# Kernel tuning notes

Measured on AMD Instinct MI355X. Metric: run time of the kernel, lower is better.

The kernel has to match this reference:

```python
import jax, jax.numpy as jnp
import numpy as np

B, L, K, D, V = 512, 50, 32, 100, 100000


def setup_inputs() -> dict:
    key = jax.random.key(0)
    ks = jax.random.split(key, 32)
    g = lambda i, shape, s=0.1: jax.random.normal(ks[i], shape, jnp.float32) * s
    lens = jax.random.randint(ks[0], (B,), 1, L + 1)
    seq = jax.random.randint(ks[1], (B, L), 1, V)
    seq = jnp.where(jnp.arange(L)[None, :] < lens[:, None], seq, 0)  # pad past lens with 0
    nei = jax.random.randint(ks[2], (B, K), 1, V)
    wei = jax.random.uniform(ks[3], (B, K), jnp.float32)
    s_vec = g(4, (B, D), 1.0)
    zp = lambda E: E.at[0].set(0.0)  # padding_idx=0
    return {
        'seq': seq, 'lens': lens, 'nei': nei, 'wei': wei, 's_vec': s_vec,
        'E_tag': zp(g(5, (V, D))), 'E_ggnn': zp(g(6, (V, D))), 'E_glob': zp(g(7, (V, D))),
        'W_ih': g(8, (2 * D, 3 * D)), 'b_ih': g(9, (3 * D,)),
        'W_hh': g(10, (D, 3 * D)), 'b_hh': g(11, (3 * D,)),
        'Wout_w': g(12, (D, D)), 'Wout_b': g(13, (D,)),
        'W_w': g(14, (D, D)),
        'W3_w': g(15, (3 * D, D)), 'W3_b': g(16, (D,)),
        'W1_w': g(17, (D + 1, D)), 'W1_b': g(18, (D,)),
        'q1_w': g(19, (D,)),
        'W2_w': g(20, (2 * D, D)), 'W2_b': g(21, (D,)),
        'G1_w': g(22, (D + 1, D)), 'G1_b': g(23, (D,)),
        'G2_w': g(24, (D, 1)), 'G2_b': g(25, (1,)),
    }


def _forward(seq, lens, nei, wei, s_vec, E_tag, E_ggnn, E_glob, W_ih, b_ih, W_hh, b_hh,
             Wout_w, Wout_b, W_w, W3_w, W3_b, W1_w, W1_b, q1_w, W2_w, W2_b,
             G1_w, G1_b, G2_w, G2_b):
    Bv, Lv = seq.shape
    # --- TAGNN_Base: vectorized chain adjacency (edges i->i+1 for i < lens-1, plus identity) ---
    i = jnp.arange(Lv - 1)
    edge = (i[None, :] < (lens - 1)[:, None]).astype(jnp.float32)  # [B, L-1]
    eye = jnp.eye(Lv, dtype=jnp.float32)[None]
    z3 = jnp.zeros((Bv, Lv, Lv), jnp.float32)
    adj_out = z3.at[:, i, i + 1].set(edge) + eye
    adj_in = z3.at[:, i + 1, i].set(edge) + eye
    # --- GGNN: one propagation step + GRUCell ---
    x = E_ggnn[seq]  # [B, L, D]
    a = jnp.concatenate([jnp.einsum('bij,bjd->bid', adj_out, x),
                         jnp.einsum('bij,bjd->bid', adj_in, x)], -1)  # [B, L, 2D]
    gi = a @ W_ih + b_ih
    gh = x @ W_hh + b_hh
    ir, iz, ig = jnp.split(gi, 3, -1)
    hr, hz, hg = jnp.split(gh, 3, -1)
    r = jax.nn.sigmoid(ir + hr)
    zt = jax.nn.sigmoid(iz + hz)
    n = jnp.tanh(ig + r * hg)
    h = (1.0 - zt) * n + zt * x
    h = h @ Wout_w + Wout_b  # [B, L, D]
    # --- target-aware attention readout ---
    mask = (seq > 0).astype(jnp.float32)
    bi = jnp.arange(Bv)
    h_last = h[bi, lens - 1]
    target = seq[bi, lens - 1]
    t_emb = E_tag[target]
    att = jax.nn.softmax(jnp.sum(h * (t_emb @ W_w)[:, None, :], -1), -1)
    h_glb = jnp.sum(h * att[..., None] * mask[..., None], 1)
    sess = jnp.tanh(jnp.concatenate([h_glb, h_last, t_emb], -1) @ W3_w + W3_b)
    logits_base = sess @ E_tag.T  # [B, V]
    # --- GlobalEncoder (2 layers); nei/wei are layer-invariant so attention msg is too ---
    h_nei = E_glob[nei]  # [B, K, D]
    feat = jnp.concatenate([h_nei * s_vec[:, None, :], wei[..., None]], -1)  # [B, K, D+1]
    score = jnp.tanh(feat @ W1_w + W1_b) @ q1_w  # [B, K]
    attg = jax.nn.softmax(score, -1)
    msg = jnp.sum(attg[..., None] * h_nei, 1)  # [B, D]
    xg = E_glob[target]
    for _ in range(2):
        xg = jax.nn.relu(jnp.concatenate([xg, msg], -1) @ W2_w + W2_b)
    # pos_emb[:, 0, :] is the scalar (L-1)/L, so h_global is scaled by 1/L
    xg = xg * (1.0 - (Lv - 1) / Lv)
    # --- gating between base logits mean and global rep ---
    mean_b = jnp.mean(logits_base, 1, keepdims=True)  # [B, 1]
    gate_in = jnp.concatenate([mean_b, xg], -1)  # [B, D+1]
    gate = jax.nn.sigmoid(jnp.tanh(gate_in @ G1_w + G1_b) @ G2_w + G2_b)  # [B, 1]
    sess2 = gate * xg + (1.0 - gate) * mean_b  # [B, D]
    return sess2 @ E_tag.T  # [B, V]


def reference(seq, lens, nei, wei, s_vec, E_tag, E_ggnn, E_glob, W_ih, b_ih, W_hh, b_hh,
              Wout_w, Wout_b, W_w, W3_w, W3_b, W1_w, W1_b, q1_w, W2_w, W2_b,
              G1_w, G1_b, G2_w, G2_b):
    return _forward(seq, lens, nei, wei, s_vec, E_tag, E_ggnn, E_glob, W_ih, b_ih, W_hh,
                    b_hh, Wout_w, Wout_b, W_w, W3_w, W3_b, W1_w, W1_b, q1_w, W2_w, W2_b,
                    G1_w, G1_b, G2_w, G2_b)
```

## Files before the change

kernel.cpp:

```cpp
#include <hip/hip_runtime.h>
#include <math.h>

namespace {
constexpr int NB = 512;
constexpr int NL = 50;
constexpr int NKN = 32;
constexpr int ND = 100;
constexpr int NV = 100000;
constexpr int NBL = NB * NL;
constexpr int NVP = 100096;
constexpr int NEB = 1564;
}

typedef __attribute__((ext_vector_type(8))) short bf16x8;
typedef __attribute__((ext_vector_type(4))) short short4v;
typedef __attribute__((ext_vector_type(8))) short short8v;
typedef __attribute__((ext_vector_type(4))) float f32x4;

__device__ inline unsigned short f2bf(float x) {
    unsigned u = __float_as_uint(x);
    unsigned r = (u + 0x7fffu + ((u >> 16) & 1u)) >> 16;
    return (unsigned short)r;
}
__device__ inline float bf2f(unsigned short h) {
    return __uint_as_float(((unsigned)h) << 16);
}

__global__ __launch_bounds__(256) void prep_E(
    const float* __restrict__ E_tag,
    unsigned short* __restrict__ Efrag,
    float* __restrict__ partialT)
{
    __shared__ float es[64][100];
    const int tid = threadIdx.x;
    const int blk = blockIdx.x;
    const int v0  = blk * 64;

    for (int idx = tid; idx < 1600; idx += 256) {
        size_t base = (size_t)v0 * 100 + (size_t)idx * 4;
        float4 e = make_float4(0.f, 0.f, 0.f, 0.f);
        if (base + 3 < (size_t)NV * ND) e = *(const float4*)(E_tag + base);
        int row = idx / 25, c4 = (idx - row * 25) * 4;
        es[row][c4]     = e.x;
        es[row][c4 + 1] = e.y;
        es[row][c4 + 2] = e.z;
        es[row][c4 + 3] = e.w;
    }
    __syncthreads();

    if (tid < ND) {
        float a = 0.f;
#pragma unroll 8
        for (int rr = 0; rr < 64; ++rr) a += es[rr][tid];
        partialT[(size_t)tid * NEB + blk] = a;
    }

    for (int idx = tid; idx < 16 * 64; idx += 256) {
        int kg = idx >> 6, vloc = idx & 63;
        short8v o;
#pragma unroll
        for (int j = 0; j < 8; ++j) {
            int k = kg * 8 + j;
            o[j] = (short)((k < ND) ? f2bf(es[vloc][k]) : 0);
        }
        *(short8v*)(Efrag + ((size_t)kg * NVP + v0 + vloc) * 8) = o;
    }
}

__global__ __launch_bounds__(256) void ebar_final(const float* __restrict__ partialT,
                                                  float* __restrict__ ebar)
{
    const int d = blockIdx.x;
    const int tid = threadIdx.x;
    float a = 0.f;
    for (int i = tid; i < NEB; i += 256) a += partialT[(size_t)d * NEB + i];
#pragma unroll
    for (int off = 32; off > 0; off >>= 1) a += __shfl_down(a, off);
    __shared__ float wsum[4];
    if ((tid & 63) == 0) wsum[tid >> 6] = a;
    __syncthreads();
    if (tid == 0)
        ebar[d] = (wsum[0] + wsum[1] + wsum[2] + wsum[3]) * (1.f / (float)NV);
}

__global__ __launch_bounds__(256) void prep_A(
    const int* __restrict__ seq, const int* __restrict__ lens,
    const float* __restrict__ E_ggnn, unsigned short* __restrict__ Afrag)
{
    __shared__ float xs[34][100];
    __shared__ float eo_s[34], ei_s[34];
    const int tid = threadIdx.x;
    const int r0  = blockIdx.x * 32;

    for (int idx = tid; idx < 34 * 25; idx += 256) {
        int row = idx / 25, qq = idx - row * 25;
        int rg = r0 - 1 + row;
        rg = rg < 0 ? 0 : (rg >= NBL ? NBL - 1 : rg);
        float4 e = *(const float4*)(E_ggnn + (size_t)seq[rg] * ND + 4 * qq);
        xs[row][4 * qq]     = e.x;
        xs[row][4 * qq + 1] = e.y;
        xs[row][4 * qq + 2] = e.z;
        xs[row][4 * qq + 3] = e.w;
    }
    for (int rr = tid; rr < 34; rr += 256) {
        int rg = r0 - 1 + rr;
        int rc = rg < 0 ? 0 : (rg >= NBL ? NBL - 1 : rg);
        int b = rc / NL, l = rc - b * NL;
        int lenb = lens[b];
        eo_s[rr] = (l < lenb - 1) ? 1.f : 0.f;
        ei_s[rr] = (l >= 1 && l <= lenb - 1) ? 1.f : 0.f;
    }
    __syncthreads();

    for (int idx = tid; idx < 32 * 48; idx += 256) {
        int rloc = idx / 48, kg = idx - rloc * 48;
        int seg = kg >> 4, kk = kg & 15;
        short8v o;
        float eo = eo_s[1 + rloc], ei = ei_s[1 + rloc];
#pragma unroll
        for (int j = 0; j < 8; ++j) {
            int k = kk * 8 + j;
            float v = 0.f;
            if (k < 100) {
                if (seg == 0)      v = xs[1 + rloc][k] + eo * xs[2 + rloc][k];
                else if (seg == 1) v = xs[1 + rloc][k] + ei * xs[rloc][k];
                else               v = xs[1 + rloc][k];
            }
            o[j] = (short)f2bf(v);
        }
        *(short8v*)(Afrag + ((size_t)kg * NBL + r0 + rloc) * 8) = o;
    }
}

__global__ __launch_bounds__(256) void prep_B(
    const float* __restrict__ W_ih, const float* __restrict__ W_hh,
    unsigned short* __restrict__ Bfrag)
{
    int idx = blockIdx.x * 256 + threadIdx.x;
    if (idx >= 48 * 640) return;
    int kg = idx / 640, col = idx - kg * 640;
    int seg = kg >> 4, kk = kg & 15;
    short8v o;
#pragma unroll
    for (int j = 0; j < 8; ++j) {
        int k = kk * 8 + j;
        float v = 0.f;
        if (k < 100) {
            if (seg == 0 && col < 300)                 v = W_ih[k * 300 + col];
            else if (seg == 1 && col < 300)            v = W_ih[(100 + k) * 300 + col];
            else if (seg == 2 && col >= 300 && col < 600) v = W_hh[k * 300 + (col - 300)];
        }
        o[j] = (short)f2bf(v);
    }
    *(short8v*)(Bfrag + (size_t)idx * 8) = o;
}

__global__ __launch_bounds__(256) void gates_mfma(
    const unsigned short* __restrict__ Afrag,
    const unsigned short* __restrict__ Bfrag,
    unsigned short* __restrict__ G)
{
    const int tid = threadIdx.x;
    const int r0  = blockIdx.x * 128;
    const int v0  = blockIdx.y * 128;
    const int lane = tid & 63;
    const int wv = tid >> 6;
    const int wm = wv >> 1, wn = wv & 1;
    const int q = lane >> 4, c = lane & 15;

    f32x4 acc[4][4];
#pragma unroll
    for (int fm = 0; fm < 4; ++fm)
#pragma unroll
        for (int fn = 0; fn < 4; ++fn) acc[fm][fn] = (f32x4)0.f;

    const bf16x8* Ap = (const bf16x8*)Afrag;
    const bf16x8* Bp = (const bf16x8*)Bfrag;

#pragma unroll
    for (int s = 0; s < 12; ++s) {
        const int kg = 4 * s + q;
        bf16x8 a[4], b[4];
#pragma unroll
        for (int fm = 0; fm < 4; ++fm)
            a[fm] = Ap[(size_t)kg * NBL + r0 + wm * 64 + fm * 16 + c];
#pragma unroll
        for (int fn = 0; fn < 4; ++fn)
            b[fn] = Bp[(size_t)kg * 640 + v0 + wn * 64 + fn * 16 + c];
#pragma unroll
        for (int fm = 0; fm < 4; ++fm)
#pragma unroll
            for (int fn = 0; fn < 4; ++fn)
                acc[fm][fn] = __builtin_amdgcn_mfma_f32_16x16x32_bf16(
                    a[fm], b[fn], acc[fm][fn], 0, 0, 0);
    }

#pragma unroll
    for (int fm = 0; fm < 4; ++fm) {
        int rb = r0 + wm * 64 + fm * 16 + q * 4;
#pragma unroll
        for (int fn = 0; fn < 4; ++fn) {
            int col = v0 + wn * 64 + fn * 16 + c;
            if (col < 600) {
#pragma unroll
                for (int r = 0; r < 4; ++r)
                    G[(size_t)(rb + r) * 600 + col] = f2bf(acc[fm][fn][r]);
            }
        }
    }
}

__global__ __launch_bounds__(256) void gru2(
    const int* __restrict__ seq, const float* __restrict__ E_ggnn,
    const unsigned short* __restrict__ G,
    const float* __restrict__ b_ih, const float* __restrict__ b_hh,
    float* __restrict__ h0)
{
    int idx = blockIdx.x * 256 + threadIdx.x;
    if (idx >= NBL * ND) return;
    int r = idx / ND, d = idx - r * ND;
    const unsigned short* Gr = G + (size_t)r * 600;
    float ir = bf2f(Gr[d])       + b_ih[d];
    float iz = bf2f(Gr[100 + d]) + b_ih[100 + d];
    float ig = bf2f(Gr[200 + d]) + b_ih[200 + d];
    float hr = bf2f(Gr[300 + d]) + b_hh[d];
    float hz = bf2f(Gr[400 + d]) + b_hh[100 + d];
    float hg = bf2f(Gr[500 + d]) + b_hh[200 + d];
    float x  = E_ggnn[(size_t)seq[r] * ND + d];
    float rg = 1.f / (1.f + expf(-(ir + hr)));
    float zg = 1.f / (1.f + expf(-(iz + hz)));
    float ng = tanhf(ig + rg * hg);
    h0[idx] = (1.f - zg) * ng + zg * x;
}

__global__ __launch_bounds__(128) void fuse_kernel(
    const int* __restrict__ seq, const int* __restrict__ lens,
    const int* __restrict__ nei, const float* __restrict__ wei,
    const float* __restrict__ s_vec, const float* __restrict__ E_tag,
    const float* __restrict__ E_glob,
    const float* __restrict__ Wout_w, const float* __restrict__ Wout_b,
    const float* __restrict__ W_w,
    const float* __restrict__ W3_w, const float* __restrict__ W3_b,
    const float* __restrict__ W1_w, const float* __restrict__ W1_b,
    const float* __restrict__ q1_w,
    const float* __restrict__ W2_w, const float* __restrict__ W2_b,
    const float* __restrict__ G1_w, const float* __restrict__ G1_b,
    const float* __restrict__ G2_w, const float* __restrict__ G2_b,
    const float* __restrict__ ebar, const float* __restrict__ h0,
    unsigned short* __restrict__ A_hi)
{
    const int b = blockIdx.x, tid = threadIdx.x;
    __shared__ float t_emb[100], tw[100], twW[100], red[128];
    __shared__ float al[50], att[50];
    __shared__ float g0[100], cc[300], sess_s[100];
    __shared__ float sv[100], hnei[32][100], msg[100], xg[100], xg2[100];
    __shared__ float attg[32], score[32];
    __shared__ float scalars[4];

    int lenb   = lens[b];
    int last_r = b * NL + (lenb - 1);
    int target = seq[last_r];

    if (tid < ND) {
        t_emb[tid] = E_tag[(size_t)target * ND + tid];
        sv[tid]    = s_vec[b * ND + tid];
    }
    __syncthreads();

    if (tid < ND) {
        float a = 0.f;
        for (int k = 0; k < ND; ++k) a += t_emb[k] * W_w[k * ND + tid];
        tw[tid] = a;
    }
    __syncthreads();

    if (tid < ND) {
        float a = 0.f;
        for (int d = 0; d < ND; ++d) a += Wout_w[tid * ND + d] * tw[d];
        twW[tid] = a;
    }
    red[tid] = (tid < ND) ? Wout_b[tid] * tw[tid] : 0.f;
    __syncthreads();
    for (int s = 64; s > 0; s >>= 1) { if (tid < s) red[tid] += red[tid + s]; __syncthreads(); }
    if (tid == 0) scalars[0] = red[0];
    __syncthreads();

    if (tid < NL) {
        const float* hr = h0 + (size_t)(b * NL + tid) * ND;
        float a = scalars[0];
        for (int k = 0; k < ND; ++k) a += hr[k] * twW[k];
        al[tid] = a;
    }
    __syncthreads();
    if (tid == 0) {
        float m = -1e30f;
        for (int l = 0; l < NL; ++l) m = fmaxf(m, al[l]);
        float s = 0.f;
        for (int l = 0; l < NL; ++l) { float e = expf(al[l] - m); att[l] = e; s += e; }
        float inv = 1.f / s, sm = 0.f;
        for (int l = 0; l < NL; ++l) { att[l] *= inv; if (l < lenb) sm += att[l]; }
        scalars[1] = sm;
    }
    __syncthreads();

    if (tid < ND) {
        float a = 0.f;
        for (int l = 0; l < lenb; ++l) a += att[l] * h0[(size_t)(b * NL + l) * ND + tid];
        g0[tid] = a;
    }
    __syncthreads();
    if (tid < ND) {
        float hg = 0.f, hl = 0.f;
        const float* hlast = h0 + (size_t)last_r * ND;
        for (int k = 0; k < ND; ++k) {
            float w = Wout_w[k * ND + tid];
            hg += g0[k] * w;
            hl += hlast[k] * w;
        }
        cc[tid]        = hg + scalars[1] * Wout_b[tid];
        cc[100 + tid]  = hl + Wout_b[tid];
        cc[200 + tid]  = t_emb[tid];
    }
    __syncthreads();

    if (tid < ND) {
        float a = W3_b[tid];
        for (int j = 0; j < 300; ++j) a += cc[j] * W3_w[j * ND + tid];
        sess_s[tid] = tanhf(a);
    }
    __syncthreads();
    red[tid] = (tid < ND) ? sess_s[tid] * ebar[tid] : 0.f;
    __syncthreads();
    for (int s = 64; s > 0; s >>= 1) { if (tid < s) red[tid] += red[tid + s]; __syncthreads(); }
    if (tid == 0) scalars[2] = red[0];
    __syncthreads();

    for (int idx = tid; idx < NKN * ND; idx += 128) {
        int k = idx / ND, d = idx - k * ND;
        hnei[k][d] = E_glob[(size_t)nei[b * NKN + k] * ND + d];
    }
    __syncthreads();

    {
        const int wv = tid >> 6, lane = tid & 63;
        for (int k2 = 0; k2 < NKN / 2; ++k2) {
            int k = k2 * 2 + wv;
            float p = 0.f;
            if (lane < 50) {
                float wk = wei[b * NKN + k];
                float a0 = W1_b[lane]      + wk * W1_w[100 * ND + lane];
                float a1 = W1_b[lane + 50] + wk * W1_w[100 * ND + lane + 50];
                for (int j = 0; j < ND; ++j) {
                    float t = hnei[k][j] * sv[j];
                    a0 += t * W1_w[j * ND + lane];
                    a1 += t * W1_w[j * ND + lane + 50];
                }
                p = tanhf(a0) * q1_w[lane] + tanhf(a1) * q1_w[lane + 50];
            }
            for (int off = 32; off > 0; off >>= 1) p += __shfl_down(p, off);
            if (lane == 0) score[k] = p;
        }
    }
    __syncthreads();

    if (tid == 0) {
        float m = -1e30f;
        for (int k = 0; k < NKN; ++k) m = fmaxf(m, score[k]);
        float s = 0.f;
        for (int k = 0; k < NKN; ++k) { float e = expf(score[k] - m); attg[k] = e; s += e; }
        float inv = 1.f / s;
        for (int k = 0; k < NKN; ++k) attg[k] *= inv;
    }
    __syncthreads();
    if (tid < ND) {
        float a = 0.f;
        for (int k = 0; k < NKN; ++k) a += attg[k] * hnei[k][tid];
        msg[tid] = a;
        xg[tid]  = E_glob[(size_t)target * ND + tid];
    }
    __syncthreads();
    if (tid < ND) {
        float a = W2_b[tid];
        for (int j = 0; j < ND; ++j) a += xg[j]  * W2_w[j * ND + tid];
        for (int j = 0; j < ND; ++j) a += msg[j] * W2_w[(100 + j) * ND + tid];
        xg2[tid] = fmaxf(a, 0.f);
    }
    __syncthreads();
    const float SCALE = (float)(1.0 - 49.0 / 50.0);
    if (tid < ND) {
        float a = W2_b[tid];
        for (int j = 0; j < ND; ++j) a += xg2[j] * W2_w[j * ND + tid];
        for (int j = 0; j < ND; ++j) a += msg[j] * W2_w[(100 + j) * ND + tid];
        xg[tid] = fmaxf(a, 0.f) * SCALE;
    }
    __syncthreads();

    if (tid < ND) {
        float a = G1_b[tid] + scalars[2] * G1_w[tid];
        for (int j = 0; j < ND; ++j) a += xg[j] * G1_w[(1 + j) * ND + tid];
        red[tid] = tanhf(a) * G2_w[tid];
    } else red[tid] = 0.f;
    __syncthreads();
    for (int s = 64; s > 0; s >>= 1) { if (tid < s) red[tid] += red[tid + s]; __syncthreads(); }
    if (tid == 0) scalars[3] = 1.f / (1.f + expf(-(red[0] + G2_b[0])));
    __syncthreads();

    {
        float val = 0.f;
        if (tid < ND) {
            float g = scalars[3];
            val = g * xg[tid] + (1.f - g) * scalars[2];
        }
        int kgrp = tid >> 3, j = tid & 7;
        A_hi[kgrp * 4096 + b * 8 + j] = f2bf(val);
    }
}

__global__ __launch_bounds__(256) void out_gemm_mfma(
    const unsigned short* __restrict__ A_hi,
    const unsigned short* __restrict__ Efrag,
    float* __restrict__ out)
{
    const int tid = threadIdx.x;
    const int v0  = blockIdx.x * 128;
    const int b0  = blockIdx.y * 128;
    const int lane = tid & 63;
    const int wv = tid >> 6;
    const int wm = wv >> 1, wn = wv & 1;
    const int q = lane >> 4, c = lane & 15;

    f32x4 acc[4][4];
#pragma unroll
    for (int fm = 0; fm < 4; ++fm)
#pragma unroll
        for (int fn = 0; fn < 4; ++fn) acc[fm][fn] = (f32x4)0.f;

    const bf16x8* Ah = (const bf16x8*)A_hi;
    const bf16x8* Ef = (const bf16x8*)Efrag;

#pragma unroll
    for (int s = 0; s < 4; ++s) {
        const int kg = 4 * s + q;
        bf16x8 a[4], b[4];
#pragma unroll
        for (int fm = 0; fm < 4; ++fm)
            a[fm] = Ah[kg * 512 + b0 + wm * 64 + fm * 16 + c];
#pragma unroll
        for (int fn = 0; fn < 4; ++fn)
            b[fn] = Ef[(size_t)kg * NVP + v0 + wn * 64 + fn * 16 + c];
#pragma unroll
        for (int fm = 0; fm < 4; ++fm)
#pragma unroll
            for (int fn = 0; fn < 4; ++fn)
                acc[fm][fn] = __builtin_amdgcn_mfma_f32_16x16x32_bf16(
                    a[fm], b[fn], acc[fm][fn], 0, 0, 0);
    }

#pragma unroll
    for (int fm = 0; fm < 4; ++fm) {
        int row_base = b0 + wm * 64 + fm * 16 + q * 4;
#pragma unroll
        for (int fn = 0; fn < 4; ++fn) {
            int col = v0 + wn * 64 + fn * 16 + c;
            if (col < NV) {
#pragma unroll
                for (int r = 0; r < 4; ++r)
                    out[(size_t)(row_base + r) * NV + col] = acc[fm][fn][r];
            }
        }
    }
}

extern "C" void kernel_launch(void* const* d_in, const int* in_sizes, int n_in,
                              void* d_out, int out_size, void* d_ws, size_t ws_size,
                              hipStream_t stream)
{
    const int*   seq    = (const int*)  d_in[0];
    const int*   lens   = (const int*)  d_in[1];
    const int*   nei    = (const int*)  d_in[2];
    const float* wei    = (const float*)d_in[3];
    const float* s_vec  = (const float*)d_in[4];
    const float* E_tag  = (const float*)d_in[5];
    const float* E_ggnn = (const float*)d_in[6];
    const float* E_glob = (const float*)d_in[7];
    const float* W_ih   = (const float*)d_in[8];
    const float* b_ih   = (const float*)d_in[9];
    const float* W_hh   = (const float*)d_in[10];
    const float* b_hh   = (const float*)d_in[11];
    const float* Wout_w = (const float*)d_in[12];
    const float* Wout_b = (const float*)d_in[13];
    const float* W_w    = (const float*)d_in[14];
    const float* W3_w   = (const float*)d_in[15];
    const float* W3_b   = (const float*)d_in[16];
    const float* W1_w   = (const float*)d_in[17];
    const float* W1_b   = (const float*)d_in[18];
    const float* q1_w   = (const float*)d_in[19];
    const float* W2_w   = (const float*)d_in[20];
    const float* W2_b   = (const float*)d_in[21];
    const float* G1_w   = (const float*)d_in[22];
    const float* G1_b   = (const float*)d_in[23];
    const float* G2_w   = (const float*)d_in[24];
    const float* G2_b   = (const float*)d_in[25];

    float* out = (float*)d_out;
    unsigned short* Gm    = (unsigned short*)out;
    unsigned short* Afrag = (unsigned short*)(out + 16000000);
    unsigned short* Bfrag = (unsigned short*)(out + 21000000);

    float* ws       = (float*)d_ws;
    float* h0       = ws;
    float* partialT = ws + 2560000;
    float* ebar     = ws + 2720000;
    unsigned short* A_hi  = (unsigned short*)(ws + 2724000);
    unsigned short* Efrag = (unsigned short*)(ws + 3000000);

    prep_E<<<NEB, 256, 0, stream>>>(E_tag, Efrag, partialT);
    ebar_final<<<ND, 256, 0, stream>>>(partialT, ebar);
    prep_A<<<NBL / 32, 256, 0, stream>>>(seq, lens, E_ggnn, Afrag);
    prep_B<<<(48 * 640 + 255) / 256, 256, 0, stream>>>(W_ih, W_hh, Bfrag);
    gates_mfma<<<dim3(NBL / 128, 5), 256, 0, stream>>>(Afrag, Bfrag, Gm);
    gru2<<<(NBL * ND + 255) / 256, 256, 0, stream>>>(seq, E_ggnn, Gm, b_ih, b_hh, h0);
    fuse_kernel<<<NB, 128, 0, stream>>>(seq, lens, nei, wei, s_vec, E_tag, E_glob,
                                        Wout_w, Wout_b, W_w, W3_w, W3_b,
                                        W1_w, W1_b, q1_w, W2_w, W2_b,
                                        G1_w, G1_b, G2_w, G2_b, ebar, h0, A_hi);
    out_gemm_mfma<<<dim3(NVP / 128, NB / 128), 256, 0, stream>>>(A_hi, Efrag, out);
}
```

Measured before the change: 220.3 us.

## Fuse gate GEMM with GRU epilogue and merge prep kernels into one launch

Combines the three preprocessing kernels (E_tag fragmenting, A fragment building, weight fragment packing) into a single launch whose blocks branch by index range. The gate GEMM is restructured so each block computes all six gate columns for a 16-wide slice of D and applies the GRU cell in registers. This removes the 25600x600 bf16 gate intermediate and its round trip through memory. It also saves two launches and keeps the gates in fp32 rather than rounding them to bf16. In exchange it does redundant MFMA work on padded columns and launches only a small grid of 400 blocks.

```diff
diff --git a/kernel.cpp b/kernel.cpp
--- a/kernel.cpp
+++ b/kernel.cpp
@@ -10,10 +10,12 @@
 constexpr int NBL = NB * NL;
 constexpr int NVP = 100096;
 constexpr int NEB = 1564;
+constexpr int NAB = 800;
+constexpr int NB2FRAG = 7 * 144 * 16;
+constexpr int NB2BLK = (NB2FRAG + 255) / 256;
 }
 
 typedef __attribute__((ext_vector_type(8))) short bf16x8;
-typedef __attribute__((ext_vector_type(4))) short short4v;
 typedef __attribute__((ext_vector_type(8))) short short8v;
 typedef __attribute__((ext_vector_type(4))) float f32x4;
 
@@ -26,44 +28,124 @@
     return __uint_as_float(((unsigned)h) << 16);
 }
 
-__global__ __launch_bounds__(256) void prep_E(
-    const float* __restrict__ E_tag,
-    unsigned short* __restrict__ Efrag,
-    float* __restrict__ partialT)
+__global__ __launch_bounds__(256) void mega_prep(
+    const float* __restrict__ E_tag, unsigned short* __restrict__ Efrag,
+    float* __restrict__ partialT,
+    const int* __restrict__ seq, const int* __restrict__ lens,
+    const float* __restrict__ E_ggnn, unsigned short* __restrict__ Afrag,
+    const float* __restrict__ W_ih, const float* __restrict__ W_hh,
+    unsigned short* __restrict__ B2)
 {
-    __shared__ float es[64][100];
+    __shared__ __align__(16) char shbuf[25856];
     const int tid = threadIdx.x;
     const int blk = blockIdx.x;
-    const int v0  = blk * 64;
-
-    for (int idx = tid; idx < 1600; idx += 256) {
-        size_t base = (size_t)v0 * 100 + (size_t)idx * 4;
-        float4 e = make_float4(0.f, 0.f, 0.f, 0.f);
-        if (base + 3 < (size_t)NV * ND) e = *(const float4*)(E_tag + base);
-        int row = idx / 25, c4 = (idx - row * 25) * 4;
-        es[row][c4]     = e.x;
-        es[row][c4 + 1] = e.y;
-        es[row][c4 + 2] = e.z;
-        es[row][c4 + 3] = e.w;
-    }
-    __syncthreads();
-
-    if (tid < ND) {
-        float a = 0.f;
+
+    if (blk < NEB) {
+        float (*es)[100] = (float(*)[100])shbuf;
+        const int v0 = blk * 64;
+        for (int idx = tid; idx < 1600; idx += 256) {
+            size_t base = (size_t)v0 * 100 + (size_t)idx * 4;
+            float4 e = make_float4(0.f, 0.f, 0.f, 0.f);
+            if (base + 3 < (size_t)NV * ND) e = *(const float4*)(E_tag + base);
+            int row = idx / 25, c4 = (idx - row * 25) * 4;
+            es[row][c4]     = e.x;
+            es[row][c4 + 1] = e.y;
+            es[row][c4 + 2] = e.z;
+            es[row][c4 + 3] = e.w;
+        }
+        __syncthreads();
+
+        if (tid < ND) {
+            float a = 0.f;
 #pragma unroll 8
-        for (int rr = 0; rr < 64; ++rr) a += es[rr][tid];
-        partialT[(size_t)tid * NEB + blk] = a;
-    }
-
-    for (int idx = tid; idx < 16 * 64; idx += 256) {
-        int kg = idx >> 6, vloc = idx & 63;
+            for (int rr = 0; rr < 64; ++rr) a += es[rr][tid];
+            partialT[(size_t)tid * NEB + blk] = a;
+        }
+        for (int idx = tid; idx < 16 * 64; idx += 256) {
+            int kg = idx >> 6, vloc = idx & 63;
+            short8v o;
+#pragma unroll
+            for (int j = 0; j < 8; ++j) {
+                int k = kg * 8 + j;
+                o[j] = (short)((k < ND) ? f2bf(es[vloc][k]) : 0);
+            }
+            *(short8v*)(Efrag + ((size_t)kg * NVP + v0 + vloc) * 8) = o;
+        }
+    } else if (blk < NEB + NAB) {
+        float (*xs)[100] = (float(*)[100])shbuf;
+        float* eo_s = (float*)(shbuf + 13600);
+        float* ei_s = eo_s + 34;
+        const int r0 = (blk - NEB) * 32;
+
+        for (int idx = tid; idx < 34 * 25; idx += 256) {
+            int row = idx / 25, qq = idx - row * 25;
+            int rg = r0 - 1 + row;
+            rg = rg < 0 ? 0 : (rg >= NBL ? NBL - 1 : rg);
+            float4 e = *(const float4*)(E_ggnn + (size_t)seq[rg] * ND + 4 * qq);
+            xs[row][4 * qq]     = e.x;
+            xs[row][4 * qq + 1] = e.y;
+            xs[row][4 * qq + 2] = e.z;
+            xs[row][4 * qq + 3] = e.w;
+        }
+        for (int rr = tid; rr < 34; rr += 256) {
+            int rg = r0 - 1 + rr;
+            int rc = rg < 0 ? 0 : (rg >= NBL ? NBL - 1 : rg);
+            int b = rc / NL, l = rc - b * NL;
+            int lenb = lens[b];
+            eo_s[rr] = (l < lenb - 1) ? 1.f : 0.f;
+            ei_s[rr] = (l >= 1 && l <= lenb - 1) ? 1.f : 0.f;
+        }
+        __syncthreads();
+
+        for (int idx = tid; idx < 32 * 48; idx += 256) {
+            int rloc = idx / 48, kg = idx - rloc * 48;
+            int seg = kg >> 4, kk = kg & 15;
+            short8v o;
+            float eo = eo_s[1 + rloc], ei = ei_s[1 + rloc];
+#pragma unroll
+            for (int j = 0; j < 8; ++j) {
+                int k = kk * 8 + j;
+                float v = 0.f;
+                if (k < 100) {
+                    if (seg == 0)      v = xs[1 + rloc][k] + eo * xs[2 + rloc][k];
+                    else if (seg == 1) v = xs[1 + rloc][k] + ei * xs[rloc][k];
+                    else               v = xs[1 + rloc][k];
+                }
+                o[j] = (short)f2bf(v);
+            }
+            *(short8v*)(Afrag + ((size_t)kg * NBL + r0 + rloc) * 8) = o;
+        }
+    } else {
+        int idx = (blk - NEB - NAB) * 256 + tid;
+        if (idx >= NB2FRAG) return;
+        int chunk = idx / 2304;
+        int rem = idx - chunk * 2304;
+        int slot = rem >> 4, c = rem & 15;
+        int d = chunk * 16 + c;
         short8v o;
-#pragma unroll
-        for (int j = 0; j < 8; ++j) {
-            int k = kg * 8 + j;
-            o[j] = (short)((k < ND) ? f2bf(es[vloc][k]) : 0);
-        }
-        *(short8v*)(Efrag + ((size_t)kg * NVP + v0 + vloc) * 8) = o;
+        if (slot < 96) {
+            int g = slot >> 5, kg = slot & 31;
+            int seg = kg >> 4, kap0 = (kg & 15) * 8;
+#pragma unroll
+            for (int j = 0; j < 8; ++j) {
+                int kap = kap0 + j;
+                float v = (kap < 100 && d < 100)
+                          ? W_ih[(seg * 100 + kap) * 300 + g * 100 + d] : 0.f;
+                o[j] = (short)f2bf(v);
+            }
+        } else {
+            int s2 = slot - 96;
+            int g = s2 >> 4, kgp = s2 & 15;
+            int kap0 = kgp * 8;
+#pragma unroll
+            for (int j = 0; j < 8; ++j) {
+                int kap = kap0 + j;
+                float v = (kap < 100 && d < 100)
+                          ? W_hh[kap * 300 + g * 100 + d] : 0.f;
+                o[j] = (short)f2bf(v);
+            }
+        }
+        *(short8v*)(B2 + (size_t)idx * 8) = o;
     }
 }
 
@@ -83,154 +165,100 @@
         ebar[d] = (wsum[0] + wsum[1] + wsum[2] + wsum[3]) * (1.f / (float)NV);
 }
 
-__global__ __launch_bounds__(256) void prep_A(
-    const int* __restrict__ seq, const int* __restrict__ lens,
-    const float* __restrict__ E_ggnn, unsigned short* __restrict__ Afrag)
-{
-    __shared__ float xs[34][100];
-    __shared__ float eo_s[34], ei_s[34];
-    const int tid = threadIdx.x;
-    const int r0  = blockIdx.x * 32;
-
-    for (int idx = tid; idx < 34 * 25; idx += 256) {
-        int row = idx / 25, qq = idx - row * 25;
-        int rg = r0 - 1 + row;
-        rg = rg < 0 ? 0 : (rg >= NBL ? NBL - 1 : rg);
-        float4 e = *(const float4*)(E_ggnn + (size_t)seq[rg] * ND + 4 * qq);
-        xs[row][4 * qq]     = e.x;
-        xs[row][4 * qq + 1] = e.y;
-        xs[row][4 * qq + 2] = e.z;
-        xs[row][4 * qq + 3] = e.w;
-    }
-    for (int rr = tid; rr < 34; rr += 256) {
-        int rg = r0 - 1 + rr;
-        int rc = rg < 0 ? 0 : (rg >= NBL ? NBL - 1 : rg);
-        int b = rc / NL, l = rc - b * NL;
-        int lenb = lens[b];
-        eo_s[rr] = (l < lenb - 1) ? 1.f : 0.f;
-        ei_s[rr] = (l >= 1 && l <= lenb - 1) ? 1.f : 0.f;
-    }
-    __syncthreads();
-
-    for (int idx = tid; idx < 32 * 48; idx += 256) {
-        int rloc = idx / 48, kg = idx - rloc * 48;
-        int seg = kg >> 4, kk = kg & 15;
-        short8v o;
-        float eo = eo_s[1 + rloc], ei = ei_s[1 + rloc];
-#pragma unroll
-        for (int j = 0; j < 8; ++j) {
-            int k = kk * 8 + j;
-            float v = 0.f;
-            if (k < 100) {
-                if (seg == 0)      v = xs[1 + rloc][k] + eo * xs[2 + rloc][k];
-                else if (seg == 1) v = xs[1 + rloc][k] + ei * xs[rloc][k];
-                else               v = xs[1 + rloc][k];
-            }
-            o[j] = (short)f2bf(v);
-        }
-        *(short8v*)(Afrag + ((size_t)kg * NBL + r0 + rloc) * 8) = o;
-    }
-}
-
-__global__ __launch_bounds__(256) void prep_B(
-    const float* __restrict__ W_ih, const float* __restrict__ W_hh,
-    unsigned short* __restrict__ Bfrag)
-{
-    int idx = blockIdx.x * 256 + threadIdx.x;
-    if (idx >= 48 * 640) return;
-    int kg = idx / 640, col = idx - kg * 640;
-    int seg = kg >> 4, kk = kg & 15;
-    short8v o;
-#pragma unroll
-    for (int j = 0; j < 8; ++j) {
-        int k = kk * 8 + j;
-        float v = 0.f;
-        if (k < 100) {
-            if (seg == 0 && col < 300)                 v = W_ih[k * 300 + col];
-            else if (seg == 1 && col < 300)            v = W_ih[(100 + k) * 300 + col];
-            else if (seg == 2 && col >= 300 && col < 600) v = W_hh[k * 300 + (col - 300)];
-        }
-        o[j] = (short)f2bf(v);
-    }
-    *(short8v*)(Bfrag + (size_t)idx * 8) = o;
-}
-
-__global__ __launch_bounds__(256) void gates_mfma(
+__global__ __launch_bounds__(256) void gates_gru(
+    const int* __restrict__ seq,
     const unsigned short* __restrict__ Afrag,
-    const unsigned short* __restrict__ Bfrag,
-    unsigned short* __restrict__ G)
+    const unsigned short* __restrict__ B2,
+    const float* __restrict__ b_ih, const float* __restrict__ b_hh,
+    const float* __restrict__ E_ggnn,
+    float* __restrict__ h0)
 {
     const int tid = threadIdx.x;
     const int r0  = blockIdx.x * 128;
-    const int v0  = blockIdx.y * 128;
+    const int cc0 = blockIdx.y ? 4 : 0;
+    const int cc1 = blockIdx.y ? 7 : 4;
     const int lane = tid & 63;
-    const int wv = tid >> 6;
-    const int wm = wv >> 1, wn = wv & 1;
+    const int w = tid >> 6;
     const int q = lane >> 4, c = lane & 15;
 
-    f32x4 acc[4][4];
-#pragma unroll
-    for (int fm = 0; fm < 4; ++fm)
-#pragma unroll
-        for (int fn = 0; fn < 4; ++fn) acc[fm][fn] = (f32x4)0.f;
-
     const bf16x8* Ap = (const bf16x8*)Afrag;
-    const bf16x8* Bp = (const bf16x8*)Bfrag;
-
-#pragma unroll
-    for (int s = 0; s < 12; ++s) {
-        const int kg = 4 * s + q;
-        bf16x8 a[4], b[4];
-#pragma unroll
-        for (int fm = 0; fm < 4; ++fm)
-            a[fm] = Ap[(size_t)kg * NBL + r0 + wm * 64 + fm * 16 + c];
-#pragma unroll
-        for (int fn = 0; fn < 4; ++fn)
-            b[fn] = Bp[(size_t)kg * 640 + v0 + wn * 64 + fn * 16 + c];
-#pragma unroll
-        for (int fm = 0; fm < 4; ++fm)
-#pragma unroll
-            for (int fn = 0; fn < 4; ++fn)
-                acc[fm][fn] = __builtin_amdgcn_mfma_f32_16x16x32_bf16(
-                    a[fm], b[fn], acc[fm][fn], 0, 0, 0);
-    }
-
-#pragma unroll
-    for (int fm = 0; fm < 4; ++fm) {
-        int rb = r0 + wm * 64 + fm * 16 + q * 4;
-#pragma unroll
-        for (int fn = 0; fn < 4; ++fn) {
-            int col = v0 + wn * 64 + fn * 16 + c;
-            if (col < 600) {
-#pragma unroll
-                for (int r = 0; r < 4; ++r)
-                    G[(size_t)(rb + r) * 600 + col] = f2bf(acc[fm][fn][r]);
-            }
-        }
-    }
-}
-
-__global__ __launch_bounds__(256) void gru2(
-    const int* __restrict__ seq, const float* __restrict__ E_ggnn,
-    const unsigned short* __restrict__ G,
-    const float* __restrict__ b_ih, const float* __restrict__ b_hh,
-    float* __restrict__ h0)
-{
-    int idx = blockIdx.x * 256 + threadIdx.x;
-    if (idx >= NBL * ND) return;
-    int r = idx / ND, d = idx - r * ND;
-    const unsigned short* Gr = G + (size_t)r * 600;
-    float ir = bf2f(Gr[d])       + b_ih[d];
-    float iz = bf2f(Gr[100 + d]) + b_ih[100 + d];
-    float ig = bf2f(Gr[200 + d]) + b_ih[200 + d];
-    float hr = bf2f(Gr[300 + d]) + b_hh[d];
-    float hz = bf2f(Gr[400 + d]) + b_hh[100 + d];
-    float hg = bf2f(Gr[500 + d]) + b_hh[200 + d];
-    float x  = E_ggnn[(size_t)seq[r] * ND + d];
-    float rg = 1.f / (1.f + expf(-(ir + hr)));
-    float zg = 1.f / (1.f + expf(-(iz + hz)));
-    float ng = tanhf(ig + rg * hg);
-    h0[idx] = (1.f - zg) * ng + zg * x;
+    const bf16x8* Bp = (const bf16x8*)B2;
+
+    const int rowA = r0 + w * 32 + c;
+
+    int tok[8];
+#pragma unroll
+    for (int fm = 0; fm < 2; ++fm)
+#pragma unroll
+        for (int reg = 0; reg < 4; ++reg)
+            tok[fm * 4 + reg] = seq[r0 + w * 32 + fm * 16 + q * 4 + reg];
+
+    for (int cc = cc0; cc < cc1; ++cc) {
+        f32x4 acc[2][6];
+#pragma unroll
+        for (int fm = 0; fm < 2; ++fm)
+#pragma unroll
+            for (int g = 0; g < 6; ++g) acc[fm][g] = (f32x4)0.f;
+
+        const size_t bbase = (size_t)cc * 144;
+
+#pragma unroll
+        for (int st = 0; st < 8; ++st) {
+            const int kg = 4 * st + q;
+            bf16x8 a0 = Ap[(size_t)kg * NBL + rowA];
+            bf16x8 a1 = Ap[(size_t)kg * NBL + rowA + 16];
+            bf16x8 b0 = Bp[(bbase + 0 * 32 + kg) * 16 + c];
+            bf16x8 b1 = Bp[(bbase + 1 * 32 + kg) * 16 + c];
+            bf16x8 b2 = Bp[(bbase + 2 * 32 + kg) * 16 + c];
+            acc[0][0] = __builtin_amdgcn_mfma_f32_16x16x32_bf16(a0, b0, acc[0][0], 0, 0, 0);
+            acc[1][0] = __builtin_amdgcn_mfma_f32_16x16x32_bf16(a1, b0, acc[1][0], 0, 0, 0);
+            acc[0][1] = __builtin_amdgcn_mfma_f32_16x16x32_bf16(a0, b1, acc[0][1], 0, 0, 0);
+            acc[1][1] = __builtin_amdgcn_mfma_f32_16x16x32_bf16(a1, b1, acc[1][1], 0, 0, 0);
+            acc[0][2] = __builtin_amdgcn_mfma_f32_16x16x32_bf16(a0, b2, acc[0][2], 0, 0, 0);
+            acc[1][2] = __builtin_amdgcn_mfma_f32_16x16x32_bf16(a1, b2, acc[1][2], 0, 0, 0);
+        }
+#pragma unroll
+        for (int st = 0; st < 4; ++st) {
+            const int kgp = 4 * st + q;
+            const int kg  = 32 + kgp;
+            bf16x8 a0 = Ap[(size_t)kg * NBL + rowA];
+            bf16x8 a1 = Ap[(size_t)kg * NBL + rowA + 16];
+            bf16x8 b0 = Bp[(bbase + 96 + 0 * 16 + kgp) * 16 + c];
+            bf16x8 b1 = Bp[(bbase + 96 + 1 * 16 + kgp) * 16 + c];
+            bf16x8 b2 = Bp[(bbase + 96 + 2 * 16 + kgp) * 16 + c];
+            acc[0][3] = __builtin_amdgcn_mfma_f32_16x16x32_bf16(a0, b0, acc[0][3], 0, 0, 0);
+            acc[1][3] = __builtin_amdgcn_mfma_f32_16x16x32_bf16(a1, b0, acc[1][3], 0, 0, 0);
+            acc[0][4] = __builtin_amdgcn_mfma_f32_16x16x32_bf16(a0, b1, acc[0][4], 0, 0, 0);
+            acc[1][4] = __builtin_amdgcn_mfma_f32_16x16x32_bf16(a1, b1, acc[1][4], 0, 0, 0);
+            acc[0][5] = __builtin_amdgcn_mfma_f32_16x16x32_bf16(a0, b2, acc[0][5], 0, 0, 0);
+            acc[1][5] = __builtin_amdgcn_mfma_f32_16x16x32_bf16(a1, b2, acc[1][5], 0, 0, 0);
+        }
+
+        const int d = cc * 16 + c;
+        if (d < ND) {
+            const float bi0 = b_ih[d], bi1 = b_ih[100 + d], bi2 = b_ih[200 + d];
+            const float bh0 = b_hh[d], bh1 = b_hh[100 + d], bh2 = b_hh[200 + d];
+#pragma unroll
+            for (int fm = 0; fm < 2; ++fm) {
+                const int rbase = r0 + w * 32 + fm * 16 + q * 4;
+#pragma unroll
+                for (int reg = 0; reg < 4; ++reg) {
+                    const int row = rbase + reg;
+                    float ir = acc[fm][0][reg] + bi0;
+                    float iz = acc[fm][1][reg] + bi1;
+                    float ig = acc[fm][2][reg] + bi2;
+                    float hr = acc[fm][3][reg] + bh0;
+                    float hz = acc[fm][4][reg] + bh1;
+                    float hg = acc[fm][5][reg] + bh2;
+                    float x  = E_ggnn[(size_t)tok[fm * 4 + reg] * ND + d];
+                    float rg = 1.f / (1.f + expf(-(ir + hr)));
+                    float zg = 1.f / (1.f + expf(-(iz + hz)));
+                    float ng = tanhf(ig + rg * hg);
+                    h0[(size_t)row * ND + d] = (1.f - zg) * ng + zg * x;
+                }
+            }
+        }
+    }
 }
 
 __global__ __launch_bounds__(128) void fuse_kernel(
@@ -503,9 +531,8 @@
     const float* G2_b   = (const float*)d_in[25];
 
     float* out = (float*)d_out;
-    unsigned short* Gm    = (unsigned short*)out;
     unsigned short* Afrag = (unsigned short*)(out + 16000000);
-    unsigned short* Bfrag = (unsigned short*)(out + 21000000);
+    unsigned short* B2    = (unsigned short*)(out + 21000000);
 
     float* ws       = (float*)d_ws;
     float* h0       = ws;
@@ -514,12 +541,11 @@
     unsigned short* A_hi  = (unsigned short*)(ws + 2724000);
     unsigned short* Efrag = (unsigned short*)(ws + 3000000);
 
-    prep_E<<<NEB, 256, 0, stream>>>(E_tag, Efrag, partialT);
+    mega_prep<<<NEB + NAB + NB2BLK, 256, 0, stream>>>(
+        E_tag, Efrag, partialT, seq, lens, E_ggnn, Afrag, W_ih, W_hh, B2);
     ebar_final<<<ND, 256, 0, stream>>>(partialT, ebar);
-    prep_A<<<NBL / 32, 256, 0, stream>>>(seq, lens, E_ggnn, Afrag);
-    prep_B<<<(48 * 640 + 255) / 256, 256, 0, stream>>>(W_ih, W_hh, Bfrag);
-    gates_mfma<<<dim3(NBL / 128, 5), 256, 0, stream>>>(Afrag, Bfrag, Gm);
-    gru2<<<(NBL * ND + 255) / 256, 256, 0, stream>>>(seq, E_ggnn, Gm, b_ih, b_hh, h0);
+    gates_gru<<<dim3(NBL / 128, 2), 256, 0, stream>>>(seq, Afrag, B2, b_ih, b_hh,
+                                                      E_ggnn, h0);
     fuse_kernel<<<NB, 128, 0, stream>>>(seq, lens, nei, wei, s_vec, E_tag, E_glob,
                                         Wout_w, Wout_b, W_w, W3_w, W3_b,
                                         W1_w, W1_b, q1_w, W2_w, W2_b,
```

Result: faster. 206.5 us (-6.3%).
